# Optimization experiments

Measured on AMD Instinct MI355X. Metric: run time of the kernel, lower is better.

## Reference

```python
import jax, jax.numpy as jnp
import numpy as np

T, B, E, L, V = 128, 256, 1024, 1024, 95


def setup_inputs() -> dict:
    key = jax.random.key(0)
    ks = jax.random.split(key, 10)
    x = jax.random.randint(ks[0], (T, B), 0, V, dtype=jnp.int64)  # [T, B] time-major tokens
    h = jnp.zeros((B, L), dtype=jnp.float32)                       # initial hidden state
    emb = jax.random.normal(ks[1], (V, E), dtype=jnp.float32) * 0.02
    s = 1.0 / np.sqrt(E + L)
    Wf = jax.random.uniform(ks[2], (L, E + L), jnp.float32, -s, s)
    bf = jax.random.uniform(ks[3], (L,), jnp.float32, -s, s)
    Wi = jax.random.uniform(ks[4], (L, E + L), jnp.float32, -s, s)
    bi = jax.random.uniform(ks[5], (L,), jnp.float32, -s, s)
    Wo = jax.random.uniform(ks[6], (L, E + L), jnp.float32, -s, s)
    bo = jax.random.uniform(ks[7], (L,), jnp.float32, -s, s)
    Wc = jax.random.uniform(ks[8], (L, E + L), jnp.float32, -s, s)
    bc = jax.random.uniform(ks[9], (L,), jnp.float32, -s, s)
    return {"x": x, "h": h, "emb": emb, "Wf": Wf, "bf": bf, "Wi": Wi,
            "bi": bi, "Wo": Wo, "bo": bo, "Wc": Wc, "bc": bc}


def reference(x, h, emb, Wf, bf, Wi, bi, Wo, bo, Wc, bc):
    # Fuse the 4 gate linears into one [E+L, 4L] GEMM per step (same math).
    W_all = jnp.concatenate([Wf, Wi, Wo, Wc], axis=0).T  # [E+L, 4L]
    b_all = jnp.concatenate([bf, bi, bo, bc], axis=0)     # [4L]
    embedded = emb[x]                                      # [T, B, E]
    c0 = jnp.zeros_like(h)

    def step(carry, e_t):
        h, c = carry
        entry = jnp.concatenate([e_t, h], axis=1)          # [B, E+L]
        g = entry @ W_all + b_all                          # [B, 4L]
        f, i, o, cg = jnp.split(g, 4, axis=1)
        c = jax.nn.sigmoid(f) * c + jax.nn.sigmoid(i) * jnp.tanh(cg)
        h = jax.nn.sigmoid(o) * jnp.tanh(c)
        return (h, c), h

    _, hs = jax.lax.scan(step, (h, c0), embedded)
    return hs  # [T, B, L]
```

## Files before the change

kernel.cpp:

```cpp
#include <hip/hip_runtime.h>
#include <stdint.h>

constexpr int TT = 128;
constexpr int BB = 256;
constexpr int LL = 1024;
constexpr int NG = 4096;
constexpr int VV = 95;

typedef short bf16x8 __attribute__((ext_vector_type(8)));
typedef float f32x4  __attribute__((ext_vector_type(4)));

typedef __attribute__((address_space(1))) const uint32_t gu32;
typedef __attribute__((address_space(3))) uint32_t lu32;

__device__ __forceinline__ unsigned short f2bf(float f) {
    unsigned int u = __builtin_bit_cast(unsigned int, f);
    unsigned int r = (u + 0x7FFFu + ((u >> 16) & 1u)) >> 16;
    return (unsigned short)r;
}
__device__ __forceinline__ float bf2f(unsigned short h) {
    unsigned int u = ((unsigned int)h) << 16;
    return __builtin_bit_cast(float, u);
}
__device__ __forceinline__ float sigmoidf_(float x) {
    return 1.0f / (1.0f + __expf(-x));
}
__device__ __forceinline__ float tanhf_(float x) {
    return 1.0f - 2.0f / (__expf(2.0f * x) + 1.0f);
}

__global__ void prep_w_all(const float* __restrict__ Wf, const float* __restrict__ Wi,
                           const float* __restrict__ Wo, const float* __restrict__ Wc,
                           unsigned short* __restrict__ Wimg,
                           unsigned short* __restrict__ Wemb_hi,
                           unsigned short* __restrict__ Wemb_lo) {
    int idx = blockIdx.x * 256 + threadIdx.x;
    const int total = NG * 2048;
    for (; idx < total; idx += gridDim.x * 256) {
        int row = idx >> 11;
        int col = idx & 2047;
        int lt   = row >> 6;
        int nl   = row & 63;
        int gate = nl >> 4;
        int l    = lt * 16 + (nl & 15);
        const float* W = (gate == 0) ? Wf : (gate == 1) ? Wi : (gate == 2) ? Wo : Wc;
        float w = W[l * 2048 + col];
        if (col >= 1024) {
            int k = col - 1024;
            int ksl = ((k >> 3) & 3) ^ (nl & 3);
            size_t byte = (size_t)lt * 131072 + (size_t)(k >> 5) * 4096 + nl * 64
                        + (ksl << 4) + (k & 7) * 2;
            *(unsigned short*)((char*)Wimg + byte) = f2bf(w);
        } else {
            unsigned short hi = f2bf(w);
            float lo = w - bf2f(hi);
            Wemb_hi[row * 1024 + col] = hi;
            Wemb_lo[row * 1024 + col] = f2bf(lo);
        }
    }
}

__global__ void prep_emb_split(const float* __restrict__ emb,
                               unsigned short* __restrict__ Eh,
                               unsigned short* __restrict__ El) {
    int idx = blockIdx.x * 256 + threadIdx.x;
    int v = idx >> 10;
    float w = (v < VV) ? emb[idx] : 0.0f;
    unsigned short hi = f2bf(w);
    Eh[idx] = hi;
    El[idx] = f2bf(w - bf2f(hi));
}

__global__ __launch_bounds__(128)
void gate_pre_mfma(const unsigned short* __restrict__ Eh, const unsigned short* __restrict__ El,
                   const unsigned short* __restrict__ Wh, const unsigned short* __restrict__ Wl,
                   const float* __restrict__ bfv, const float* __restrict__ biv,
                   const float* __restrict__ bov, const float* __restrict__ bcv,
                   float* __restrict__ gp2) {
    const int lt   = blockIdx.x;
    const int tid  = threadIdx.x;
    const int lane = tid & 63;
    const int wm   = tid >> 6;
    const int l15  = lane & 15;
    const int kq   = lane >> 4;

    f32x4 acc[3][4];
    #pragma unroll
    for (int mf = 0; mf < 3; ++mf)
        #pragma unroll
        for (int nf = 0; nf < 4; ++nf) acc[mf][nf] = (f32x4){0.f, 0.f, 0.f, 0.f};

    #pragma unroll 2
    for (int ks = 0; ks < 32; ++ks) {
        const int k0 = ks * 32 + kq * 8;
        bf16x8 ah[3], al[3], bh[4], bl[4];
        #pragma unroll
        for (int mf = 0; mf < 3; ++mf) {
            const size_t ao = (size_t)(wm * 48 + mf * 16 + l15) * 1024 + k0;
            ah[mf] = *(const bf16x8*)(Eh + ao);
            al[mf] = *(const bf16x8*)(El + ao);
        }
        #pragma unroll
        for (int nf = 0; nf < 4; ++nf) {
            const size_t bo = (size_t)(lt * 64 + nf * 16 + l15) * 1024 + k0;
            bh[nf] = *(const bf16x8*)(Wh + bo);
            bl[nf] = *(const bf16x8*)(Wl + bo);
        }
        #pragma unroll
        for (int mf = 0; mf < 3; ++mf)
            #pragma unroll
            for (int nf = 0; nf < 4; ++nf) {
                acc[mf][nf] = __builtin_amdgcn_mfma_f32_16x16x32_bf16(ah[mf], bh[nf], acc[mf][nf], 0, 0, 0);
                acc[mf][nf] = __builtin_amdgcn_mfma_f32_16x16x32_bf16(ah[mf], bl[nf], acc[mf][nf], 0, 0, 0);
                acc[mf][nf] = __builtin_amdgcn_mfma_f32_16x16x32_bf16(al[mf], bh[nf], acc[mf][nf], 0, 0, 0);
            }
    }

    const int lgl = lt * 16 + l15;
    #pragma unroll
    for (int nf = 0; nf < 4; ++nf) {
        const float* bias = (nf == 0) ? bfv : (nf == 1) ? biv : (nf == 2) ? bov : bcv;
        const float bv = bias[lgl];
        #pragma unroll
        for (int mf = 0; mf < 3; ++mf)
            #pragma unroll
            for (int r = 0; r < 4; ++r) {
                const int v = wm * 48 + mf * 16 + kq * 4 + r;
                if (v < VV)
                    gp2[((size_t)v * LL + lgl) * 4 + nf] = acc[mf][nf][r] + bv;
            }
    }
}

__global__ void init_state(const float* __restrict__ h_init,
                           unsigned short* __restrict__ h0,
                           unsigned int* __restrict__ flags) {
    int idx = blockIdx.x * 256 + threadIdx.x;
    h0[idx] = f2bf(h_init[idx]);
    if (idx < 4096) flags[idx] = 0;
}

__global__ __launch_bounds__(256, 1)
void lstm_all3(const unsigned short* __restrict__ Wimg,
               const float* __restrict__ gp2,
               const int* __restrict__ x,
               unsigned short* __restrict__ hb0,
               unsigned short* __restrict__ hb1,
               float* __restrict__ out,
               unsigned int* __restrict__ flags) {
    __shared__ unsigned short wlds_s[65536];
    char* wlds = (char*)wlds_s;

    const int tid  = threadIdx.x;
    const int lane = tid & 63;
    const int wv   = tid >> 6;
    const int bt   = blockIdx.x >> 6;
    const int lt   = blockIdx.x & 63;
    const int l15  = lane & 15;
    const int kq   = lane >> 4;

    const int l  = lt * 16 + l15;
    const int b0 = bt * 64 + wv * 16 + kq * 4;

    {
        const char* wsrc = (const char*)Wimg + (size_t)lt * 131072 + tid * 16;
        #pragma unroll
        for (int j = 0; j < 32; ++j)
            __builtin_amdgcn_global_load_lds((gu32*)(wsrc + j * 4096),
                                             (lu32*)(wlds + j * 4096 + wv * 1024),
                                             16, 0, 0);
        asm volatile("s_waitcnt vmcnt(0)" ::: "memory");
        __syncthreads();
    }
    const char* bbase = wlds + l15 * 64 + ((kq ^ (l15 & 3)) << 4);

    const size_t arow = (size_t)(bt * 64 + wv * 16 + l15) * 2048 + kq * 16;
    const char* aptr0 = (const char*)hb0 + arow;
    const char* aptr1 = (const char*)hb1 + arow;
    const unsigned int* fpoll = flags + (((bt << 6) + lane) << 4);
    const int myflag = ((bt << 6) + lt) << 4;

    float c_r[4] = {0.f, 0.f, 0.f, 0.f};
    float* out_t = out;

    #define SB __builtin_amdgcn_sched_barrier(0);

    #define POLLALL()                                                            \
        { unsigned int fv;                                                       \
          for (;;) {                                                             \
            asm volatile("global_load_dword %0, %1, off sc0 sc1\n\t"             \
                         "s_waitcnt vmcnt(0)"                                    \
                         : "=&v"(fv) : "v"(fpoll) : "memory");                   \
            if (__all((int)(fv >= (unsigned int)t))) break;                      \
            __builtin_amdgcn_s_sleep(1);                                         \
          } }

    #define ISSUEA(buf, q)                                                       \
        _Pragma("unroll") for (int ki = 0; ki < 8; ++ki) {                       \
            const char* ap = aptr + ((q) * 8 + ki) * 64;                         \
            asm volatile("global_load_dwordx4 %0, %1, off sc0 sc1"               \
                         : "=&v"(buf[ki]) : "v"(ap));                            \
        }

    #define QCOMP(areg, q)                                                       \
        _Pragma("unroll") for (int ki = 0; ki < 8; ++ki) {                       \
            const int ks = (q) * 8 + ki;                                         \
            const char* bc = bbase + ks * 4096;                                  \
            bf16x8 bw0 = *(const bf16x8*)(bc);                                   \
            bf16x8 bw1 = *(const bf16x8*)(bc + 1024);                            \
            bf16x8 bw2 = *(const bf16x8*)(bc + 2048);                            \
            bf16x8 bw3 = *(const bf16x8*)(bc + 3072);                            \
            acc[0] = __builtin_amdgcn_mfma_f32_16x16x32_bf16(areg[ki], bw0, acc[0], 0, 0, 0); \
            acc[1] = __builtin_amdgcn_mfma_f32_16x16x32_bf16(areg[ki], bw1, acc[1], 0, 0, 0); \
            acc[2] = __builtin_amdgcn_mfma_f32_16x16x32_bf16(areg[ki], bw2, acc[2], 0, 0, 0); \
            acc[3] = __builtin_amdgcn_mfma_f32_16x16x32_bf16(areg[ki], bw3, acc[3], 0, 0, 0); \
        }

    #define WAITV(N) asm volatile("s_waitcnt vmcnt(" #N ")" ::: "memory");

    for (int t = 0; t < TT; ++t) {
        const char* aptr = (t & 1) ? aptr1 : aptr0;
        unsigned short* hout = (t & 1) ? hb0 : hb1;
        const int* xt = x + t * BB;

        f32x4 acc[4];
        #pragma unroll
        for (int nf = 0; nf < 4; ++nf) acc[nf] = (f32x4){0.f, 0.f, 0.f, 0.f};
        bf16x8 bufA[8], bufB[8];

        POLLALL()
        SB

        int4 xv;
        {
            const int* xp = xt + b0;
            asm volatile("global_load_dwordx4 %0, %1, off"
                         : "=&v"(xv) : "v"(xp));
        }
        ISSUEA(bufA, 0)
        ISSUEA(bufB, 1)
        SB
        WAITV(8)
        SB
        float4 gpv[4];
        {
            const int vr[4] = {xv.x, xv.y, xv.z, xv.w};
            #pragma unroll
            for (int r = 0; r < 4; ++r) {
                const float* gpp = gp2 + ((size_t)vr[r] * LL + l) * 4;
                asm volatile("global_load_dwordx4 %0, %1, off"
                             : "=&v"(gpv[r]) : "v"(gpp));
            }
        }
        SB
        QCOMP(bufA, 0) SB
        ISSUEA(bufA, 2) SB
        WAITV(12)
        SB
        QCOMP(bufB, 1) SB
        ISSUEA(bufB, 3) SB
        WAITV(8)
        SB
        QCOMP(bufA, 2) SB
        WAITV(0)
        SB
        QCOMP(bufB, 3)

        float hnew[4];
        #pragma unroll
        for (int r = 0; r < 4; ++r) {
            const float gf = acc[0][r] + gpv[r].x;
            const float gi = acc[1][r] + gpv[r].y;
            const float go = acc[2][r] + gpv[r].z;
            const float gc = acc[3][r] + gpv[r].w;
            const float cn = sigmoidf_(gf) * c_r[r] + sigmoidf_(gi) * tanhf_(gc);
            hnew[r] = sigmoidf_(go) * tanhf_(cn);
            c_r[r] = cn;
        }
        #pragma unroll
        for (int r = 0; r < 4; ++r) {
            const size_t off = (size_t)(b0 + r) * LL + l;
            unsigned int hbits = f2bf(hnew[r]);
            const unsigned short* hp = hout + off;
            asm volatile("global_store_short %0, %1, off sc0 sc1"
                         :: "v"(hp), "v"(hbits) : "memory");
        }
        #pragma unroll
        for (int r = 0; r < 4; ++r)
            out_t[(size_t)(b0 + r) * LL + l] = hnew[r];

        WAITV(4)
        __syncthreads();
        if (t < TT - 1 && tid == 0)
            atomicExch(&flags[myflag], (unsigned int)(t + 1));
        out_t += BB * LL;
    }

    #undef SB
    #undef POLLALL
    #undef ISSUEA
    #undef QCOMP
    #undef WAITV
}

extern "C" void kernel_launch(void* const* d_in, const int* in_sizes, int n_in,
                              void* d_out, int out_size, void* d_ws, size_t ws_size,
                              hipStream_t stream) {
    const int*   x      = (const int*)d_in[0];
    const float* h_init = (const float*)d_in[1];
    const float* emb    = (const float*)d_in[2];
    const float* Wf     = (const float*)d_in[3];
    const float* bfv    = (const float*)d_in[4];
    const float* Wi     = (const float*)d_in[5];
    const float* biv    = (const float*)d_in[6];
    const float* Wo     = (const float*)d_in[7];
    const float* bov    = (const float*)d_in[8];
    const float* Wc     = (const float*)d_in[9];
    const float* bcv    = (const float*)d_in[10];
    float* out = (float*)d_out;

    char* ws = (char*)d_ws;
    unsigned short* Wimg    = (unsigned short*)(ws);
    unsigned short* Wemb_hi = (unsigned short*)(ws + 8388608);
    unsigned short* Wemb_lo = (unsigned short*)(ws + 16777216);
    unsigned short* Eh      = (unsigned short*)(ws + 25165824);
    unsigned short* El      = (unsigned short*)(ws + 25362432);
    float*          gp2     = (float*)(ws + 25559040);
    unsigned short* hb0     = (unsigned short*)(ws + 27131904);
    unsigned short* hb1     = (unsigned short*)(ws + 27656192);
    unsigned int*   flags   = (unsigned int*)(ws + 28180480);

    prep_w_all<<<4096, 256, 0, stream>>>(Wf, Wi, Wo, Wc, Wimg, Wemb_hi, Wemb_lo);
    prep_emb_split<<<384, 256, 0, stream>>>(emb, Eh, El);
    gate_pre_mfma<<<64, 128, 0, stream>>>(Eh, El, Wemb_hi, Wemb_lo,
                                          bfv, biv, bov, bcv, gp2);
    init_state<<<1024, 256, 0, stream>>>(h_init, hb0, flags);

    void* kargs[] = {(void*)&Wimg, (void*)&gp2, (void*)&x,
                     (void*)&hb0, (void*)&hb1, (void*)&out, (void*)&flags};
    hipLaunchCooperativeKernel(reinterpret_cast<void*>(lstm_all3),
                               dim3(256), dim3(256), kargs, 0, stream);
}
```

Before: 965.2 us.

## Switch recurrent GEMM to 32x32x16 MFMA with LDS gate transpose and prefetch

Reworks the per-step recurrent matmul from four 16x16x32 MFMAs per k-slice to one 32x32x16 MFMA per wave on a 2x2 wave tiling, with a new swizzled weight image layout. Accumulators are staged through a shared-memory buffer so each thread gathers its four gates for the elementwise update. The A loads are deepened to eight pipelined groups, the next step's token gate-preactivation loads are prefetched, and flag polling is moved to a single wave followed by a barrier. This aims to cut LDS weight reads and MFMA issue overhead, at the cost of an extra LDS round trip and barrier per step.

```diff
diff --git a/kernel.cpp b/kernel.cpp
--- a/kernel.cpp
+++ b/kernel.cpp
@@ -7,8 +7,9 @@
 constexpr int NG = 4096;
 constexpr int VV = 95;
 
-typedef short bf16x8 __attribute__((ext_vector_type(8)));
-typedef float f32x4  __attribute__((ext_vector_type(4)));
+typedef short bf16x8  __attribute__((ext_vector_type(8)));
+typedef float f32x4   __attribute__((ext_vector_type(4)));
+typedef float f32x16  __attribute__((ext_vector_type(16)));
 
 typedef __attribute__((address_space(1))) const uint32_t gu32;
 typedef __attribute__((address_space(3))) uint32_t lu32;
@@ -42,15 +43,19 @@
         int lt   = row >> 6;
         int nl   = row & 63;
         int gate = nl >> 4;
-        int l    = lt * 16 + (nl & 15);
+        int l15  = nl & 15;
+        int l    = lt * 16 + l15;
         const float* W = (gate == 0) ? Wf : (gate == 1) ? Wi : (gate == 2) ? Wo : Wc;
         float w = W[l * 2048 + col];
         if (col >= 1024) {
             int k = col - 1024;
-            int ksl = ((k >> 3) & 3) ^ (nl & 3);
-            size_t byte = (size_t)lt * 131072 + (size_t)(k >> 5) * 4096 + nl * 64
-                        + (ksl << 4) + (k & 7) * 2;
-            *(unsigned short*)((char*)Wimg + byte) = f2bf(w);
+            int n_local = l15 * 4 + gate;
+            int ks = k >> 4;
+            int khalf = (k >> 3) & 1;
+            int j = k & 7;
+            int g = n_local * 2 + khalf;
+            int gp = g ^ ((g >> 3) & 7);
+            Wimg[(size_t)lt * 65536 + ks * 1024 + gp * 8 + j] = f2bf(w);
         } else {
             unsigned short hi = f2bf(w);
             float lo = w - bf2f(hi);
@@ -141,7 +146,7 @@
 }
 
 __global__ __launch_bounds__(256, 1)
-void lstm_all3(const unsigned short* __restrict__ Wimg,
+void lstm_all4(const unsigned short* __restrict__ Wimg,
                const float* __restrict__ gp2,
                const int* __restrict__ x,
                unsigned short* __restrict__ hb0,
@@ -149,18 +154,23 @@
                float* __restrict__ out,
                unsigned int* __restrict__ flags) {
     __shared__ unsigned short wlds_s[65536];
+    __shared__ float g_s[64 * 66 + 8];
     char* wlds = (char*)wlds_s;
 
     const int tid  = threadIdx.x;
     const int lane = tid & 63;
     const int wv   = tid >> 6;
+    const int wm   = wv >> 1;
+    const int wn   = wv & 1;
     const int bt   = blockIdx.x >> 6;
     const int lt   = blockIdx.x & 63;
-    const int l15  = lane & 15;
-    const int kq   = lane >> 4;
-
-    const int l  = lt * 16 + l15;
-    const int b0 = bt * 64 + wv * 16 + kq * 4;
+    const int c31  = lane & 31;
+    const int kh   = lane >> 5;
+
+    const int l15r = tid & 15;
+    const int m0   = (tid >> 4) * 4;
+    const int le   = lt * 16 + l15r;
+    const int b0   = bt * 64 + m0;
 
     {
         const char* wsrc = (const char*)Wimg + (size_t)lt * 131072 + tid * 16;
@@ -172,9 +182,15 @@
         asm volatile("s_waitcnt vmcnt(0)" ::: "memory");
         __syncthreads();
     }
-    const char* bbase = wlds + l15 * 64 + ((kq ^ (l15 & 3)) << 4);
-
-    const size_t arow = (size_t)(bt * 64 + wv * 16 + l15) * 2048 + kq * 16;
+
+    int boff;
+    {
+        const int g = (wn * 32 + c31) * 2 + kh;
+        boff = (g ^ ((g >> 3) & 7)) * 16;
+    }
+    const char* bbase = wlds + boff;
+
+    const size_t arow = (size_t)(bt * 64 + wm * 32 + c31) * 2048 + kh * 16;
     const char* aptr0 = (const char*)hb0 + arow;
     const char* aptr1 = (const char*)hb1 + arow;
     const unsigned int* fpoll = flags + (((bt << 6) + lane) << 4);
@@ -184,102 +200,119 @@
     float* out_t = out;
 
     #define SB __builtin_amdgcn_sched_barrier(0);
-
-    #define POLLALL()                                                            \
-        { unsigned int fv;                                                       \
-          for (;;) {                                                             \
-            asm volatile("global_load_dword %0, %1, off sc0 sc1\n\t"             \
-                         "s_waitcnt vmcnt(0)"                                    \
-                         : "=&v"(fv) : "v"(fpoll) : "memory");                   \
-            if (__all((int)(fv >= (unsigned int)t))) break;                      \
-            __builtin_amdgcn_s_sleep(1);                                         \
-          } }
-
-    #define ISSUEA(buf, q)                                                       \
+    #define WAITV(N) { asm volatile("s_waitcnt vmcnt(" #N ")" ::: "memory"); SB }
+
+    #define ISSUEA(buf, g)                                                       \
         _Pragma("unroll") for (int ki = 0; ki < 8; ++ki) {                       \
-            const char* ap = aptr + ((q) * 8 + ki) * 64;                         \
+            const char* ap = aptr + ((g) * 8 + ki) * 32;                         \
             asm volatile("global_load_dwordx4 %0, %1, off sc0 sc1"               \
                          : "=&v"(buf[ki]) : "v"(ap));                            \
-        }
-
-    #define QCOMP(areg, q)                                                       \
+        } SB
+
+    #define QCOMP(areg, g)                                                       \
         _Pragma("unroll") for (int ki = 0; ki < 8; ++ki) {                       \
-            const int ks = (q) * 8 + ki;                                         \
-            const char* bc = bbase + ks * 4096;                                  \
-            bf16x8 bw0 = *(const bf16x8*)(bc);                                   \
-            bf16x8 bw1 = *(const bf16x8*)(bc + 1024);                            \
-            bf16x8 bw2 = *(const bf16x8*)(bc + 2048);                            \
-            bf16x8 bw3 = *(const bf16x8*)(bc + 3072);                            \
-            acc[0] = __builtin_amdgcn_mfma_f32_16x16x32_bf16(areg[ki], bw0, acc[0], 0, 0, 0); \
-            acc[1] = __builtin_amdgcn_mfma_f32_16x16x32_bf16(areg[ki], bw1, acc[1], 0, 0, 0); \
-            acc[2] = __builtin_amdgcn_mfma_f32_16x16x32_bf16(areg[ki], bw2, acc[2], 0, 0, 0); \
-            acc[3] = __builtin_amdgcn_mfma_f32_16x16x32_bf16(areg[ki], bw3, acc[3], 0, 0, 0); \
-        }
-
-    #define WAITV(N) asm volatile("s_waitcnt vmcnt(" #N ")" ::: "memory");
+            const int ks = (g) * 8 + ki;                                         \
+            bf16x8 bw = *(const bf16x8*)(bbase + ks * 2048);                     \
+            acc = __builtin_amdgcn_mfma_f32_32x32x16_bf16(areg[ki], bw, acc, 0, 0, 0); \
+        } SB
+
+    float4 gpv[4];
+    {
+        int4 xv0;
+        const int* xp0 = x + b0;
+        asm volatile("global_load_dwordx4 %0, %1, off" : "=&v"(xv0) : "v"(xp0));
+        WAITV(0)
+        const int vr[4] = {xv0.x, xv0.y, xv0.z, xv0.w};
+        #pragma unroll
+        for (int r = 0; r < 4; ++r) {
+            const float* gpp = gp2 + ((size_t)vr[r] * LL + le) * 4;
+            asm volatile("global_load_dwordx4 %0, %1, off" : "=&v"(gpv[r]) : "v"(gpp));
+        }
+        WAITV(0)
+    }
 
     for (int t = 0; t < TT; ++t) {
         const char* aptr = (t & 1) ? aptr1 : aptr0;
         unsigned short* hout = (t & 1) ? hb0 : hb1;
-        const int* xt = x + t * BB;
-
-        f32x4 acc[4];
-        #pragma unroll
-        for (int nf = 0; nf < 4; ++nf) acc[nf] = (f32x4){0.f, 0.f, 0.f, 0.f};
-        bf16x8 bufA[8], bufB[8];
-
-        POLLALL()
+
+        if (wv == 0) {
+            unsigned int fv;
+            for (;;) {
+                asm volatile("global_load_dword %0, %1, off sc0 sc1\n\t"
+                             "s_waitcnt vmcnt(0)"
+                             : "=&v"(fv) : "v"(fpoll) : "memory");
+                if (__all((int)(fv >= (unsigned int)t))) break;
+                __builtin_amdgcn_s_sleep(2);
+            }
+        }
+        __syncthreads();
         SB
 
-        int4 xv;
+        f32x16 acc;
+        #pragma unroll
+        for (int e = 0; e < 16; ++e) acc[e] = 0.f;
+        bf16x8 aA[8], aB[8];
+
+        int4 xvn;
         {
-            const int* xp = xt + b0;
-            asm volatile("global_load_dwordx4 %0, %1, off"
-                         : "=&v"(xv) : "v"(xp));
-        }
-        ISSUEA(bufA, 0)
-        ISSUEA(bufB, 1)
-        SB
+            const int tn = (t + 1 < TT) ? t + 1 : t;
+            const int* xpn = x + tn * BB + b0;
+            asm volatile("global_load_dwordx4 %0, %1, off" : "=&v"(xvn) : "v"(xpn));
+        }
+        ISSUEA(aA, 0)
+        ISSUEA(aB, 1)
         WAITV(8)
-        SB
-        float4 gpv[4];
+        QCOMP(aA, 0) ISSUEA(aA, 2) WAITV(8)
+        QCOMP(aB, 1) ISSUEA(aB, 3) WAITV(8)
+        QCOMP(aA, 2) ISSUEA(aA, 4) WAITV(8)
+        QCOMP(aB, 3) ISSUEA(aB, 5) WAITV(8)
+        QCOMP(aA, 4) ISSUEA(aA, 6) WAITV(8)
+        QCOMP(aB, 5) ISSUEA(aB, 7) WAITV(8)
+        QCOMP(aA, 6)
+        float4 gpn[4];
         {
-            const int vr[4] = {xv.x, xv.y, xv.z, xv.w};
+            const int vr[4] = {xvn.x, xvn.y, xvn.z, xvn.w};
             #pragma unroll
             for (int r = 0; r < 4; ++r) {
-                const float* gpp = gp2 + ((size_t)vr[r] * LL + l) * 4;
-                asm volatile("global_load_dwordx4 %0, %1, off"
-                             : "=&v"(gpv[r]) : "v"(gpp));
+                const float* gpp = gp2 + ((size_t)vr[r] * LL + le) * 4;
+                asm volatile("global_load_dwordx4 %0, %1, off" : "=&v"(gpn[r]) : "v"(gpp));
             }
         }
         SB
-        QCOMP(bufA, 0) SB
-        ISSUEA(bufA, 2) SB
-        WAITV(12)
-        SB
-        QCOMP(bufB, 1) SB
-        ISSUEA(bufB, 3) SB
-        WAITV(8)
-        SB
-        QCOMP(bufA, 2) SB
-        WAITV(0)
-        SB
-        QCOMP(bufB, 3)
+        WAITV(4)
+        QCOMP(aB, 7)
+
+        {
+            const int fcol = (wn * 32 + c31) * 66 + wm * 32 + kh * 4;
+            #pragma unroll
+            for (int q = 0; q < 4; ++q) {
+                *(float4*)&g_s[fcol + q * 8] =
+                    (float4){acc[4 * q + 0], acc[4 * q + 1], acc[4 * q + 2], acc[4 * q + 3]};
+            }
+        }
+        __syncthreads();
+
+        float gvv[4][4];
+        #pragma unroll
+        for (int gate = 0; gate < 4; ++gate) {
+            const float4 q0 = *(const float4*)&g_s[(l15r * 4 + gate) * 66 + m0];
+            gvv[gate][0] = q0.x; gvv[gate][1] = q0.y; gvv[gate][2] = q0.z; gvv[gate][3] = q0.w;
+        }
 
         float hnew[4];
         #pragma unroll
         for (int r = 0; r < 4; ++r) {
-            const float gf = acc[0][r] + gpv[r].x;
-            const float gi = acc[1][r] + gpv[r].y;
-            const float go = acc[2][r] + gpv[r].z;
-            const float gc = acc[3][r] + gpv[r].w;
+            const float gf = gvv[0][r] + gpv[r].x;
+            const float gi = gvv[1][r] + gpv[r].y;
+            const float go = gvv[2][r] + gpv[r].z;
+            const float gc = gvv[3][r] + gpv[r].w;
             const float cn = sigmoidf_(gf) * c_r[r] + sigmoidf_(gi) * tanhf_(gc);
             hnew[r] = sigmoidf_(go) * tanhf_(cn);
             c_r[r] = cn;
         }
         #pragma unroll
         for (int r = 0; r < 4; ++r) {
-            const size_t off = (size_t)(b0 + r) * LL + l;
+            const size_t off = (size_t)(b0 + r) * LL + le;
             unsigned int hbits = f2bf(hnew[r]);
             const unsigned short* hp = hout + off;
             asm volatile("global_store_short %0, %1, off sc0 sc1"
@@ -287,20 +320,22 @@
         }
         #pragma unroll
         for (int r = 0; r < 4; ++r)
-            out_t[(size_t)(b0 + r) * LL + l] = hnew[r];
+            out_t[(size_t)(b0 + r) * LL + le] = hnew[r];
 
         WAITV(4)
         __syncthreads();
         if (t < TT - 1 && tid == 0)
             atomicExch(&flags[myflag], (unsigned int)(t + 1));
+
+        #pragma unroll
+        for (int r = 0; r < 4; ++r) gpv[r] = gpn[r];
         out_t += BB * LL;
     }
 
     #undef SB
-    #undef POLLALL
+    #undef WAITV
     #undef ISSUEA
     #undef QCOMP
-    #undef WAITV
 }
 
 extern "C" void kernel_launch(void* const* d_in, const int* in_sizes, int n_in,
@@ -338,6 +373,6 @@
 
     void* kargs[] = {(void*)&Wimg, (void*)&gp2, (void*)&x,
                      (void*)&hb0, (void*)&hb1, (void*)&out, (void*)&flags};
-    hipLaunchCooperativeKernel(reinterpret_cast<void*>(lstm_all3),
+    hipLaunchCooperativeKernel(reinterpret_cast<void*>(lstm_all4),
                                dim3(256), dim3(256), kargs, 0, stream);
 }
```

Measured after the change: 1.521 ms. 57.6% more time.
